# Optimization experiments

Measured on AMD Instinct MI355X. Metric: run time of the kernel, lower is better.

Reference implementation:

```python
import jax, jax.numpy as jnp
import numpy as np
import itertools

VOXEL_SIZE = np.array([0.05, 0.05, 0.1], np.float32)   # xyz, from cfg.voxel_size
GRID_OFFSET = np.array([0.0, -40.0, -3.0], np.float32)  # xyz, cfg.grid_bounds[:3]
BN_EPS = 1e-3

# ---------------- rulebook construction (numpy, mirrors spconv indice pairs) ----------------

def _enc(c, shape):
    Z, Y, X = shape
    c = c.astype(np.int64)
    return ((c[:, 0] * Z + c[:, 1]) * Y + c[:, 2]) * X + c[:, 3]

def _lookup(sk, order, q):
    pos = np.clip(np.searchsorted(sk, q), 0, len(sk) - 1)
    return np.where((q >= 0) & (sk[pos] == q), order[pos], -1).astype(np.int32)

def _subm_rulebook(coords, shape):
    # submanifold conv k=3, pad=1: output sites == input sites; neighbor = out + (k-1)
    keys = _enc(coords, shape)
    order = np.argsort(keys).astype(np.int32)
    sk = keys[order]
    dims = np.array(shape)
    rows = []
    for off in itertools.product((-1, 0, 1), repeat=3):
        nb = coords[:, 1:] + np.array(off)
        inb = ((nb >= 0) & (nb < dims)).all(1)
        full = np.concatenate([coords[:, :1], nb], 1)
        q = np.where(inb, _enc(full, shape), -1)
        rows.append(_lookup(sk, order, q))
    return np.stack(rows)  # [27, N] input index or -1

def _strided_rulebook(coords, shape_in, ksize, stride, pad):
    # regular sparse conv: out active = any site receiving a contribution; in = out*s - p + k
    ksize = np.array(ksize); stride = np.array(stride); pad = np.array(pad)
    shape_out = tuple((((np.array(shape_in) + 2 * pad - ksize) // stride) + 1).tolist())
    keys = _enc(coords, shape_in)
    order = np.argsort(keys).astype(np.int32)
    sk = keys[order]
    cand = []
    for k in itertools.product(*[range(int(x)) for x in ksize]):
        num = coords[:, 1:] + pad - np.array(k)
        ok = (num % stride == 0).all(1)
        o = num // stride
        ok &= (o >= 0).all(1) & (o < np.array(shape_out)).all(1)
        cand.append(np.concatenate([coords[ok, :1], o[ok]], 1))
    out_coords = np.unique(np.concatenate(cand, 0), axis=0).astype(np.int32)
    dims_in = np.array(shape_in)
    rows = []
    for k in itertools.product(*[range(int(x)) for x in ksize]):
        ic = out_coords[:, 1:] * stride - pad + np.array(k)
        inb = ((ic >= 0) & (ic < dims_in)).all(1)
        full = np.concatenate([out_coords[:, :1], ic], 1)
        q = np.where(inb, _enc(full, shape_in), -1)
        rows.append(_lookup(sk, order, q))
    return out_coords, np.stack(rows), shape_out

# ---------------- inputs ----------------

def setup_inputs() -> dict:
    rng = np.random.default_rng(0)
    B, NPB = 2, 8000
    shape0 = (41, 1600, 1280)
    parts = []
    for b in range(B):
        c = np.stack([rng.integers(0, shape0[0], 4 * NPB),
                      rng.integers(0, shape0[1], 4 * NPB),
                      rng.integers(0, shape0[2], 4 * NPB)], 1)
        c = np.unique(c, axis=0)[:NPB]
        parts.append(np.concatenate([np.full((len(c), 1), b), c], 1))
    coords0 = np.concatenate(parts, 0).astype(np.int32)

    rb0 = _subm_rulebook(coords0, shape0)
    coords1, rbc1, shape1 = _strided_rulebook(coords0, shape0, (3, 3, 3), (2, 2, 2), (1, 1, 1))
    rb1 = _subm_rulebook(coords1, shape1)
    coords2, rbc2, shape2 = _strided_rulebook(coords1, shape1, (3, 3, 3), (2, 2, 2), (1, 1, 1))
    rb2 = _subm_rulebook(coords2, shape2)
    coords3, rbc3, shape3 = _strided_rulebook(coords2, shape2, (3, 3, 3), (2, 2, 2), (0, 1, 1))
    rb3 = _subm_rulebook(coords3, shape3)
    coords4, rbc4, shape4 = _strided_rulebook(coords3, shape3, (3, 1, 1), (2, 1, 1), (0, 0, 0))

    def w(*s):
        return jnp.asarray((rng.standard_normal(s) * 0.1).astype(np.float32))

    inp = {"features": jnp.asarray(rng.standard_normal((len(coords0), 4)).astype(np.float32))}
    specs = [("1a", 27, 4, 16), ("1b", 27, 16, 16), ("1c", 27, 16, 32),
             ("2a", 27, 32, 32), ("2b", 27, 32, 32), ("2c", 27, 32, 64),
             ("3a", 27, 64, 64), ("3b", 27, 64, 64), ("3c", 27, 64, 64), ("3d", 27, 64, 64),
             ("4a", 27, 64, 64), ("4b", 27, 64, 64), ("4c", 27, 64, 64), ("4d", 3, 64, 64)]
    for name, K, ci, co in specs:
        inp["w" + name] = w(K, ci, co)
        inp["g" + name] = jnp.asarray((np.abs(rng.standard_normal(co)) + 0.5).astype(np.float32))
        inp["b" + name] = jnp.asarray((rng.standard_normal(co) * 0.1).astype(np.float32))
    inp.update(coordinates=jnp.asarray(coords0), coords1=jnp.asarray(coords1),
               coords2=jnp.asarray(coords2), coords3=jnp.asarray(coords3),
               rb0=jnp.asarray(rb0), rbc1=jnp.asarray(rbc1), rb1=jnp.asarray(rb1),
               rbc2=jnp.asarray(rbc2), rb2=jnp.asarray(rb2), rbc3=jnp.asarray(rbc3),
               rb3=jnp.asarray(rb3), rbc4=jnp.asarray(rbc4), batch_size=B)
    return inp

# ---------------- forward math ----------------

def _sconv(feat, rb, W):
    # gather-GEMM-scatter: rb[k,n] = input row feeding output n via kernel offset k (-1 = none)
    out = jnp.zeros((rb.shape[1], W.shape[2]), feat.dtype)
    for k in range(W.shape[0]):
        idx = rb[k]
        g = jnp.where(idx[:, None] >= 0, feat[jnp.clip(idx, 0)], 0.0)
        out = out + g @ W[k]
    return out

def _bn_relu(x, g, b):
    # BatchNorm1d in training mode over active voxels (biased var), eps=1e-3, then ReLU
    m = jnp.mean(x, 0)
    v = jnp.mean(jnp.square(x - m), 0)
    return jax.nn.relu((x - m) * (g / jnp.sqrt(v + BN_EPS)) + b)

def reference(features, w1a, g1a, b1a, w1b, g1b, b1b, w1c, g1c, b1c,
              w2a, g2a, b2a, w2b, g2b, b2b, w2c, g2c, b2c,
              w3a, g3a, b3a, w3b, g3b, b3b, w3c, g3c, b3c, w3d, g3d, b3d,
              w4a, g4a, b4a, w4b, g4b, b4b, w4c, g4c, b4c, w4d, g4d, b4d,
              coordinates, coords1, coords2, coords3,
              rb0, rbc1, rb1, rbc2, rb2, rbc3, rb3, rbc4, batch_size):
    f0 = features
    h = _bn_relu(_sconv(f0, rb0, w1a), g1a, b1a)
    h = _bn_relu(_sconv(h, rb0, w1b), g1b, b1b)
    f1 = _bn_relu(_sconv(h, rbc1, w1c), g1c, b1c)
    h = _bn_relu(_sconv(f1, rb1, w2a), g2a, b2a)
    h = _bn_relu(_sconv(h, rb1, w2b), g2b, b2b)
    f2 = _bn_relu(_sconv(h, rbc2, w2c), g2c, b2c)
    h = _bn_relu(_sconv(f2, rb2, w3a), g3a, b3a)
    h = _bn_relu(_sconv(h, rb2, w3b), g3b, b3b)
    h = _bn_relu(_sconv(h, rb2, w3c), g3c, b3c)
    f3 = _bn_relu(_sconv(h, rbc3, w3d), g3d, b3d)
    h = _bn_relu(_sconv(f3, rb3, w4a), g4a, b4a)
    h = _bn_relu(_sconv(h, rb3, w4b), g4b, b4b)
    h = _bn_relu(_sconv(h, rb3, w4c), g4c, b4c)
    f4 = _bn_relu(_sconv(h, rbc4, w4d), g4d, b4d)

    vs = jnp.asarray(VOXEL_SIZE)
    off = jnp.asarray(GRID_OFFSET)
    def to_global(stride, c):
        # indices are (b,z,y,x); flip -> (x,y,z,b); take xyz
        return jnp.flip(c, 1)[:, :3].astype(jnp.float32) * (vs * stride) + off
    xyz0 = to_global(1, coordinates)
    xyz1 = to_global(2, coords1)
    xyz2 = to_global(4, coords2)
    xyz3 = to_global(8, coords3)
    return (xyz0, f0, xyz1, f1, xyz2, f2, xyz3, f3, f4)
```

## Files before the change

### kernel.cpp

```cpp
#include <hip/hip_runtime.h>

#define BN_EPS 1e-3f
#define NREP 16

typedef __attribute__((ext_vector_type(8))) short short8;
typedef __attribute__((ext_vector_type(4))) float float4v;

__device__ __forceinline__ short f2bf(float f) {
    unsigned u = __float_as_uint(f);
    unsigned r = (u + 0x7FFFu + ((u >> 16) & 1u)) >> 16;
    return (short)r;
}

template <int N>
__device__ __forceinline__ void waitcnt_vm() {
    __builtin_amdgcn_s_waitcnt(0xF70 | (N & 15) | ((N >> 4) << 14));
}

__device__ __forceinline__ void wave_barrier() { asm volatile("s_barrier" ::: "memory"); }

__device__ __forceinline__ void dma16(const short* g, short* l) {
    __builtin_amdgcn_global_load_lds((const __attribute__((address_space(1))) void*)g,
                                     (__attribute__((address_space(3))) void*)l, 16, 0, 0);
}


__global__ __launch_bounds__(256) void zero_kernel(float* p, int n) {
    int i = blockIdx.x * 256 + threadIdx.x;
    if (i < n) p[i] = 0.f;
}

__global__ __launch_bounds__(256) void copy_kernel(const float* __restrict__ in,
                                                   float* __restrict__ out, int n) {
    int i = blockIdx.x * 256 + threadIdx.x;
    if (i < n) out[i] = in[i];
}

__global__ __launch_bounds__(256) void zero_rows_kernel(short* a, short* b, long maxN) {
    int t = threadIdx.x;
    if (t < 32) a[maxN * 32 + t] = 0;
    else if (t < 96) a[maxN * 64 + (t - 32)] = 0;
    else if (t < 128) b[maxN * 32 + (t - 96)] = 0;
    else if (t < 192) b[maxN * 64 + (t - 128)] = 0;
}

__global__ __launch_bounds__(256) void xyz_kernel(const int* __restrict__ coords,
                                                  float* __restrict__ out, int N,
                                                  float sx, float sy, float sz) {
    int n = blockIdx.x * 256 + threadIdx.x;
    if (n >= N) return;
    int4 c = ((const int4*)coords)[n];
    out[n * 3 + 0] = c.w * sx;
    out[n * 3 + 1] = c.z * sy - 40.0f;
    out[n * 3 + 2] = c.y * sz - 3.0f;
}

__global__ __launch_bounds__(256) void convert_f0(const float* __restrict__ f,
                                                  short* __restrict__ dst, int N) {
    int i = blockIdx.x * 256 + threadIdx.x;
    if (i >= N * 32) return;
    int c = i & 31, n = i >> 5;
    dst[i] = (c < 4) ? f2bf(f[n * 4 + c]) : (short)0;
}

struct PrepAll {
    const float* src[14];
    short* dst[14];
    int CI[14];
    int CO[14];
    int CHP[14];
    int cum[15];
};

__global__ __launch_bounds__(256) void prep_all_kernel(PrepAll d) {
    int i = blockIdx.x * 256 + threadIdx.x;
    if (i >= d.cum[14]) return;
    int l = 0;
    while (l < 13 && i >= d.cum[l + 1]) ++l;
    int f = i - d.cum[l];
    int CO = d.CO[l], CI = d.CI[l];
    int NCH = d.CHP[l] / 32, CT = CO / 16;
    int e = f & 7;
    int u = f >> 3;
    int l16 = u & 15;
    int q = (u >> 4) & 3;
    int u2 = u >> 6;
    int t = u2 % CT;
    int c = (u2 / CT) % NCH;
    int k = u2 / (CT * NCH);
    int ci = c * 32 + q * 8 + e;
    int co = t * 16 + l16;
    float v = (ci < CI) ? d.src[l][((size_t)k * CI + ci) * CO + co] : 0.f;
    d.dst[l][f] = f2bf(v);
}

struct ASet {
    short8 v0, v1, v2, v3;
};

template <int CHP, int CO, int K>
__global__ __launch_bounds__(256, 4) void sconv_hyb(const short* __restrict__ feat,
                                                    const int* __restrict__ rb,
                                                    const short* __restrict__ Wt,
                                                    float* __restrict__ out,
                                                    float* __restrict__ stats, int N, int zrow) {
    constexpr int NCH = CHP / 32;
    constexpr int CT = CO / 16;
    constexpr int BTILE = CO * CHP;
    constexpr int NB = BTILE / 512;
    constexpr int A = 2 * NCH;
    constexpr int ROWS = 128;

    __shared__ __align__(16) short ldsB[3 * BTILE];
    __shared__ int sIdx[K * ROWS];

    const int tid = threadIdx.x;
    const int w = tid >> 6;
    const int lane = tid & 63;
    const int quad = lane >> 4;
    const int l16 = lane & 15;
    const int m0 = blockIdx.x * ROWS;

    for (int e = tid; e < K * ROWS; e += 256) {
        int r = m0 + (e & (ROWS - 1));
        sIdx[e] = (r < N) ? __builtin_nontemporal_load(&rb[(size_t)(e >> 7) * N + r]) : -1;
    }
    __syncthreads();

    const short* fquad = feat + quad * 8;

    auto issueB = [&](int kp, int slot) {
        const short* wk = Wt + (size_t)kp * BTILE + lane * 8;
        short* bb = ldsB + slot * BTILE;
#pragma unroll
        for (int jj = 0; jj < (NB + 3) / 4; ++jj) {
            int j = jj * 4 + w;
            if (j < NB) dma16(wk + j * 512, bb + j * 512);
        }
    };
    auto issueA = [&](int kp) {
        ASet s;
        int i0 = sIdx[kp * ROWS + w * 32 + l16];
        int i1 = sIdx[kp * ROWS + w * 32 + 16 + l16];
        const short* p0 = fquad + (size_t)(i0 < 0 ? zrow : i0) * CHP;
        const short* p1 = fquad + (size_t)(i1 < 0 ? zrow : i1) * CHP;
        s.v0 = *(const short8*)p0;
        s.v2 = *(const short8*)p1;
        if constexpr (NCH == 2) {
            s.v1 = *(const short8*)(p0 + 32);
            s.v3 = *(const short8*)(p1 + 32);
        } else {
            s.v1 = (short8)0;
            s.v3 = (short8)0;
        }
        return s;
    };

    float4v acc[2][CT];
#pragma unroll
    for (int mt = 0; mt < 2; ++mt)
#pragma unroll
        for (int t = 0; t < CT; ++t) acc[mt][t] = (float4v)0.f;

    constexpr int BW0 = NB / 4 + ((NB % 4) > 0 ? 1 : 0);
    constexpr int BW1 = NB / 4 + ((NB % 4) > 1 ? 1 : 0);
    constexpr int BW2 = NB / 4 + ((NB % 4) > 2 ? 1 : 0);
    constexpr int BW3 = NB / 4;

    issueB(0, 0);
    ASet sA = issueA(0);
    issueB(1, 1);
    ASet sB = issueA(1);
    ASet sC;

    int slotRd = 0, slotWr = 2;
    for (int k = 0; k < K; ++k) {
        if (k < K - 1) {
            if (w == 0) waitcnt_vm<BW0 + A>();
            else if (w == 1) waitcnt_vm<BW1 + A>();
            else if (w == 2) waitcnt_vm<BW2 + A>();
            else waitcnt_vm<BW3 + A>();
        } else {
            waitcnt_vm<0>();
        }
        __builtin_amdgcn_sched_barrier(0);
        wave_barrier();
        if (k + 2 < K) {
            issueB(k + 2, slotWr);
            sC = issueA(k + 2);
        }
        const short* bb = ldsB + slotRd * BTILE;
#pragma unroll
        for (int c = 0; c < NCH; ++c) {
#pragma unroll
            for (int t = 0; t < CT; ++t) {
                short8 bf = *(const short8*)(bb + ((c * CT + t) * 64 + quad * 16 + l16) * 8);
#pragma unroll
                for (int mt = 0; mt < 2; ++mt) {
                    short8 af = (mt == 0) ? ((c == 0) ? sA.v0 : sA.v1)
                                          : ((c == 0) ? sA.v2 : sA.v3);
                    acc[mt][t] = __builtin_amdgcn_mfma_f32_16x16x32_bf16(af, bf, acc[mt][t], 0,
                                                                         0, 0);
                }
            }
        }
        sA = sB;
        sB = sC;
        slotRd = (slotRd == 2) ? 0 : slotRd + 1;
        slotWr = (slotWr == 2) ? 0 : slotWr + 1;
    }

#pragma unroll
    for (int mt = 0; mt < 2; ++mt)
#pragma unroll
        for (int t = 0; t < CT; ++t) {
            int col = t * 16 + l16;
#pragma unroll
            for (int r = 0; r < 4; ++r) {
                int orow = m0 + w * 32 + mt * 16 + quad * 4 + r;
                if (orow < N)
                    __builtin_nontemporal_store(acc[mt][t][r], &out[(size_t)orow * CO + col]);
            }
        }

    __syncthreads();
    float* red = (float*)ldsB;
#pragma unroll
    for (int t = 0; t < CT; ++t) {
        float s = 0.f, ss = 0.f;
#pragma unroll
        for (int mt = 0; mt < 2; ++mt)
#pragma unroll
            for (int r = 0; r < 4; ++r) {
                float v = acc[mt][t][r];
                s += v;
                ss += v * v;
            }
        s += __shfl_xor(s, 16);
        s += __shfl_xor(s, 32);
        ss += __shfl_xor(ss, 16);
        ss += __shfl_xor(ss, 32);
        if (lane < 16) {
            red[w * 2 * CO + t * 16 + lane] = s;
            red[w * 2 * CO + CO + t * 16 + lane] = ss;
        }
    }
    __syncthreads();
    if (tid < 2 * CO) {
        float v = red[tid] + red[2 * CO + tid] + red[4 * CO + tid] + red[6 * CO + tid];
        float* st = stats + (size_t)(blockIdx.x & (NREP - 1)) * 128;
        atomicAdd(&st[(tid < CO) ? tid : (64 + tid - CO)], v);
    }
}

template <int COUT, int CHPN, bool F32OUT, bool BFOUT>
__global__ __launch_bounds__(256) void bn_apply(const float* __restrict__ x,
                                                const float* __restrict__ stats,
                                                const float* __restrict__ g,
                                                const float* __restrict__ b,
                                                float* __restrict__ fout,
                                                short* __restrict__ bfout, int N) {
    constexpr int CW = BFOUT ? CHPN : COUT;
    __shared__ float ssc[COUT];
    __shared__ float ssh[COUT];
    int tid = threadIdx.x;
    if (tid < COUT) {
        float s = 0.f, q = 0.f;
#pragma unroll
        for (int r = 0; r < NREP; ++r) {
            s += stats[r * 128 + tid];
            q += stats[r * 128 + 64 + tid];
        }
        float inv = 1.0f / (float)N;
        float m = s * inv;
        float v = q * inv - m * m;
        float sc = g[tid] / sqrtf(v + BN_EPS);
        ssc[tid] = sc;
        ssh[tid] = b[tid] - m * sc;
    }
    __syncthreads();
    long i = (long)blockIdx.x * 256 + tid;
    if (i >= (long)N * CW) return;
    int c = (int)(i % CW);
    long n = i / CW;
    float y = 0.f;
    if (c < COUT) {
        y = fmaxf(__builtin_nontemporal_load(&x[n * COUT + c]) * ssc[c] + ssh[c], 0.f);
        if (F32OUT) __builtin_nontemporal_store(y, &fout[n * COUT + c]);
    }
    if (BFOUT) bfout[n * CHPN + c] = f2bf(y);
}


template <int CHP, int CO, int K>
static void conv(const short* fin, const int* rb, const short* wt, float* preact, float* stats,
                 int N, int zrow, hipStream_t stream) {
    dim3 grid((N + 127) / 128);
    hipLaunchKernelGGL((sconv_hyb<CHP, CO, K>), grid, dim3(256), 0, stream, fin, rb, wt, preact,
                       stats, N, zrow);
}

template <int COUT, int CHPN, bool F32OUT, bool BFOUT>
static void apply(const float* preact, const float* stats, const float* g, const float* b,
                  float* fout, short* bfout, int N, hipStream_t stream) {
    constexpr int CW = BFOUT ? CHPN : COUT;
    int blocks = (int)(((long)N * CW + 255) / 256);
    hipLaunchKernelGGL((bn_apply<COUT, CHPN, F32OUT, BFOUT>), dim3(blocks), dim3(256), 0, stream,
                       preact, stats, g, b, fout, bfout, N);
}

extern "C" void kernel_launch(void* const* d_in, const int* in_sizes, int n_in, void* d_out,
                              int out_size, void* d_ws, size_t ws_size, hipStream_t stream) {
    const float* features = (const float*)d_in[0];
    const float* W[14];
    const float* G[14];
    const float* Bb[14];
    for (int i = 0; i < 14; ++i) {
        W[i] = (const float*)d_in[1 + 3 * i];
        G[i] = (const float*)d_in[2 + 3 * i];
        Bb[i] = (const float*)d_in[3 + 3 * i];
    }
    const int* coords0 = (const int*)d_in[43];
    const int* coords1 = (const int*)d_in[44];
    const int* coords2 = (const int*)d_in[45];
    const int* coords3 = (const int*)d_in[46];
    const int* rb0 = (const int*)d_in[47];
    const int* rbc1 = (const int*)d_in[48];
    const int* rb1 = (const int*)d_in[49];
    const int* rbc2 = (const int*)d_in[50];
    const int* rb2 = (const int*)d_in[51];
    const int* rbc3 = (const int*)d_in[52];
    const int* rb3 = (const int*)d_in[53];
    const int* rbc4 = (const int*)d_in[54];

    const int N0 = in_sizes[0] / 4;
    const int N1 = in_sizes[44] / 4;
    const int N2 = in_sizes[45] / 4;
    const int N3 = in_sizes[46] / 4;
    const int N4 = in_sizes[54] / 3;

    float* out = (float*)d_out;
    long off = 0;
    float* xyz0 = out + off; off += (long)N0 * 3;
    float* f0   = out + off; off += (long)N0 * 4;
    float* xyz1 = out + off; off += (long)N1 * 3;
    float* f1   = out + off; off += (long)N1 * 32;
    float* xyz2 = out + off; off += (long)N2 * 3;
    float* f2   = out + off; off += (long)N2 * 64;
    float* xyz3 = out + off; off += (long)N3 * 3;
    float* f3   = out + off; off += (long)N3 * 64;
    float* f4   = out + off;

    long maxN = N0;
    if (N1 > maxN) maxN = N1;
    if (N2 > maxN) maxN = N2;
    if (N3 > maxN) maxN = N3;
    if (N4 > maxN) maxN = N4;
    const int zrow = (int)maxN;

    float* preact = (float*)d_ws;
    float* statsBase = preact + (size_t)maxN * 64;
    short* bfA = (short*)(statsBase + 14 * NREP * 128);
    short* bfB = bfA + (size_t)(maxN + 1) * 64;
    short* wtBase = bfB + (size_t)(maxN + 1) * 64;

    static const int KK[14] = {27, 27, 27, 27, 27, 27, 27, 27, 27, 27, 27, 27, 27, 3};
    static const int CI[14] = {4, 16, 16, 32, 32, 32, 64, 64, 64, 64, 64, 64, 64, 64};
    static const int CO[14] = {16, 16, 32, 32, 32, 64, 64, 64, 64, 64, 64, 64, 64, 64};
    short* WT[14];
    PrepAll pd;
    {
        size_t o = 0;
        int cum = 0;
        for (int l = 0; l < 14; ++l) {
            WT[l] = wtBase + o;
            int chp = CI[l] <= 32 ? 32 : 64;
            pd.src[l] = W[l];
            pd.dst[l] = WT[l];
            pd.CI[l] = CI[l];
            pd.CO[l] = CO[l];
            pd.CHP[l] = chp;
            pd.cum[l] = cum;
            cum += KK[l] * CO[l] * chp;
            o += (size_t)KK[l] * CO[l] * chp;
        }
        pd.cum[14] = cum;
    }

    int nstats = 14 * NREP * 128;
    hipLaunchKernelGGL(zero_kernel, dim3((nstats + 255) / 256), dim3(256), 0, stream, statsBase,
                       nstats);
    hipLaunchKernelGGL(zero_rows_kernel, dim3(1), dim3(256), 0, stream, bfA, bfB, maxN);
    hipLaunchKernelGGL(prep_all_kernel, dim3((pd.cum[14] + 255) / 256), dim3(256), 0, stream, pd);

    hipLaunchKernelGGL(copy_kernel, dim3((N0 * 4 + 255) / 256), dim3(256), 0, stream, features, f0,
                       N0 * 4);
    hipLaunchKernelGGL(xyz_kernel, dim3((N0 + 255) / 256), dim3(256), 0, stream, coords0, xyz0, N0,
                       0.05f, 0.05f, 0.1f);
    hipLaunchKernelGGL(xyz_kernel, dim3((N1 + 255) / 256), dim3(256), 0, stream, coords1, xyz1, N1,
                       0.1f, 0.1f, 0.2f);
    hipLaunchKernelGGL(xyz_kernel, dim3((N2 + 255) / 256), dim3(256), 0, stream, coords2, xyz2, N2,
                       0.2f, 0.2f, 0.4f);
    hipLaunchKernelGGL(xyz_kernel, dim3((N3 + 255) / 256), dim3(256), 0, stream, coords3, xyz3, N3,
                       0.4f, 0.4f, 0.8f);
    hipLaunchKernelGGL(convert_f0, dim3((N0 * 32 + 255) / 256), dim3(256), 0, stream, features,
                       bfA, N0);

    float* st = statsBase;
#define STAT(l) (st + (size_t)(l)*NREP * 128)

    conv<32, 16, 27>(bfA, rb0, WT[0], preact, STAT(0), N0, zrow, stream);
    apply<16, 32, false, true>(preact, STAT(0), G[0], Bb[0], nullptr, bfB, N0, stream);
    conv<32, 16, 27>(bfB, rb0, WT[1], preact, STAT(1), N0, zrow, stream);
    apply<16, 32, false, true>(preact, STAT(1), G[1], Bb[1], nullptr, bfA, N0, stream);
    conv<32, 32, 27>(bfA, rbc1, WT[2], preact, STAT(2), N1, zrow, stream);
    apply<32, 32, true, true>(preact, STAT(2), G[2], Bb[2], f1, bfB, N1, stream);

    conv<32, 32, 27>(bfB, rb1, WT[3], preact, STAT(3), N1, zrow, stream);
    apply<32, 32, false, true>(preact, STAT(3), G[3], Bb[3], nullptr, bfA, N1, stream);
    conv<32, 32, 27>(bfA, rb1, WT[4], preact, STAT(4), N1, zrow, stream);
    apply<32, 32, false, true>(preact, STAT(4), G[4], Bb[4], nullptr, bfB, N1, stream);
    conv<32, 64, 27>(bfB, rbc2, WT[5], preact, STAT(5), N2, zrow, stream);
    apply<64, 64, true, true>(preact, STAT(5), G[5], Bb[5], f2, bfA, N2, stream);

    conv<64, 64, 27>(bfA, rb2, WT[6], preact, STAT(6), N2, zrow, stream);
    apply<64, 64, false, true>(preact, STAT(6), G[6], Bb[6], nullptr, bfB, N2, stream);
    conv<64, 64, 27>(bfB, rb2, WT[7], preact, STAT(7), N2, zrow, stream);
    apply<64, 64, false, true>(preact, STAT(7), G[7], Bb[7], nullptr, bfA, N2, stream);
    conv<64, 64, 27>(bfA, rb2, WT[8], preact, STAT(8), N2, zrow, stream);
    apply<64, 64, false, true>(preact, STAT(8), G[8], Bb[8], nullptr, bfB, N2, stream);
    conv<64, 64, 27>(bfB, rbc3, WT[9], preact, STAT(9), N3, zrow, stream);
    apply<64, 64, true, true>(preact, STAT(9), G[9], Bb[9], f3, bfA, N3, stream);

    conv<64, 64, 27>(bfA, rb3, WT[10], preact, STAT(10), N3, zrow, stream);
    apply<64, 64, false, true>(preact, STAT(10), G[10], Bb[10], nullptr, bfB, N3, stream);
    conv<64, 64, 27>(bfB, rb3, WT[11], preact, STAT(11), N3, zrow, stream);
    apply<64, 64, false, true>(preact, STAT(11), G[11], Bb[11], nullptr, bfA, N3, stream);
    conv<64, 64, 27>(bfA, rb3, WT[12], preact, STAT(12), N3, zrow, stream);
    apply<64, 64, false, true>(preact, STAT(12), G[12], Bb[12], nullptr, bfB, N3, stream);
    conv<64, 64, 3>(bfB, rbc4, WT[13], preact, STAT(13), N4, zrow, stream);
    apply<64, 64, true, false>(preact, STAT(13), G[13], Bb[13], f4, nullptr, N4, stream);
#undef STAT
}
```

Measured before the change: 787.7 us.

## Skip kernel offsets with no active neighbors per row tile in sparse conv

Each 128-row block now scans its rulebook slice, flags which kernel offsets have any valid input index, and compacts them into a list. The software-pipelined weight and feature loads and the MFMA loop then iterate only over the active offsets, skipping weight DMA and zero-row gathers for empty offsets. Nontemporal hints on the preactivation store and its reload in the BN-apply kernel are also dropped, so the intermediate can stay in cache between kernels. This adds an extra barrier and a ballot pass, and makes the loop trip count dynamic.

Result: faster. 733.1 us (-6.9%).

```diff
diff --git a/kernel.cpp b/kernel.cpp
--- a/kernel.cpp
+++ b/kernel.cpp
@@ -113,6 +113,9 @@
 
     __shared__ __align__(16) short ldsB[3 * BTILE];
     __shared__ int sIdx[K * ROWS];
+    __shared__ int sFlag[K];
+    __shared__ int sKl[K];
+    __shared__ int sKn;
 
     const int tid = threadIdx.x;
     const int w = tid >> 6;
@@ -121,11 +124,23 @@
     const int l16 = lane & 15;
     const int m0 = blockIdx.x * ROWS;
 
+    if (tid < K) sFlag[tid] = 0;
+    __syncthreads();
     for (int e = tid; e < K * ROWS; e += 256) {
         int r = m0 + (e & (ROWS - 1));
-        sIdx[e] = (r < N) ? __builtin_nontemporal_load(&rb[(size_t)(e >> 7) * N + r]) : -1;
-    }
-    __syncthreads();
+        int v = (r < N) ? rb[(size_t)(e >> 7) * N + r] : -1;
+        sIdx[e] = v;
+        if (v >= 0) sFlag[e >> 7] = 1;
+    }
+    __syncthreads();
+    if (w == 0) {
+        int f = (lane < K) ? sFlag[lane] : 0;
+        unsigned long long m = __ballot(f != 0);
+        if (f) sKl[__popcll(m & ((1ull << lane) - 1ull))] = lane;
+        if (lane == 0) sKn = (int)__popcll(m);
+    }
+    __syncthreads();
+    const int nk = sKn;
 
     const short* fquad = feat + quad * 8;
 
@@ -167,15 +182,19 @@
     constexpr int BW2 = NB / 4 + ((NB % 4) > 2 ? 1 : 0);
     constexpr int BW3 = NB / 4;
 
-    issueB(0, 0);
-    ASet sA = issueA(0);
-    issueB(1, 1);
-    ASet sB = issueA(1);
-    ASet sC;
+    ASet sA{}, sB{}, sC{};
+    if (nk > 0) {
+        issueB(sKl[0], 0);
+        sA = issueA(sKl[0]);
+    }
+    if (nk > 1) {
+        issueB(sKl[1], 1);
+        sB = issueA(sKl[1]);
+    }
 
     int slotRd = 0, slotWr = 2;
-    for (int k = 0; k < K; ++k) {
-        if (k < K - 1) {
+    for (int i = 0; i < nk; ++i) {
+        if (i < nk - 1) {
             if (w == 0) waitcnt_vm<BW0 + A>();
             else if (w == 1) waitcnt_vm<BW1 + A>();
             else if (w == 2) waitcnt_vm<BW2 + A>();
@@ -185,9 +204,9 @@
         }
         __builtin_amdgcn_sched_barrier(0);
         wave_barrier();
-        if (k + 2 < K) {
-            issueB(k + 2, slotWr);
-            sC = issueA(k + 2);
+        if (i + 2 < nk) {
+            issueB(sKl[i + 2], slotWr);
+            sC = issueA(sKl[i + 2]);
         }
         const short* bb = ldsB + slotRd * BTILE;
 #pragma unroll
@@ -218,8 +237,7 @@
 #pragma unroll
             for (int r = 0; r < 4; ++r) {
                 int orow = m0 + w * 32 + mt * 16 + quad * 4 + r;
-                if (orow < N)
-                    __builtin_nontemporal_store(acc[mt][t][r], &out[(size_t)orow * CO + col]);
+                if (orow < N) out[(size_t)orow * CO + col] = acc[mt][t][r];
             }
         }
 
@@ -285,7 +303,7 @@
     long n = i / CW;
     float y = 0.f;
     if (c < COUT) {
-        y = fmaxf(__builtin_nontemporal_load(&x[n * COUT + c]) * ssc[c] + ssh[c], 0.f);
+        y = fmaxf(x[n * COUT + c] * ssc[c] + ssh[c], 0.f);
         if (F32OUT) __builtin_nontemporal_store(y, &fout[n * COUT + c]);
     }
     if (BFOUT) bfout[n * CHPN + c] = f2bf(y);
```
